# Optimization experiments

Hardware: AMD Instinct MI355X
Metric: run time of the kernel (lower is better)

## Reference

```python
import jax, jax.numpy as jnp
import numpy as np

V = 50000        # fine nodes
E = 400000       # edges
NEXT_DIM = 12500 # coarse nodes (nextDim)
B = 2
FIN, FOUT = 64, 128


def setup_inputs() -> dict:
    key = jax.random.key(0)
    ks = jax.random.split(key, 12)
    x = jax.random.normal(ks[0], (B, V, FIN), dtype=jnp.float32)
    adjValue = jax.random.uniform(ks[1], (E,), dtype=jnp.float32)
    edgeOne = jnp.ones((E,), dtype=jnp.float32)
    E_start = jax.random.randint(ks[2], (E,), 0, V, dtype=jnp.int32)
    E_end = jax.random.randint(ks[3], (E,), 0, V, dtype=jnp.int32)
    # avg-pool assignment: each fine node v -> coarse node v//4, weight 1/4
    fine = jnp.arange(V, dtype=jnp.int32)
    avgPoolAsgnIdx = jnp.stack([fine // 4, fine])  # [2, nnz]
    avgPoolAsgnValue = jnp.full((V,), 0.25, dtype=jnp.float32)
    s = 0.05
    W_res = jax.random.normal(ks[4], (FIN, FOUT), dtype=jnp.float32) * s
    b_res = jnp.zeros((FOUT,), dtype=jnp.float32)
    W0_self = jax.random.normal(ks[5], (FIN, FOUT), dtype=jnp.float32) * s
    W0_nb = jax.random.normal(ks[6], (FIN, FOUT), dtype=jnp.float32) * s
    b0 = jnp.zeros((FOUT,), dtype=jnp.float32)
    W1_self = jax.random.normal(ks[7], (FOUT, FOUT), dtype=jnp.float32) * s
    W1_nb = jax.random.normal(ks[8], (FOUT, FOUT), dtype=jnp.float32) * s
    b1 = jnp.zeros((FOUT,), dtype=jnp.float32)
    return {"x": x, "adjValue": adjValue, "edgeOne": edgeOne,
            "E_start": E_start, "E_end": E_end,
            "avgPoolAsgnIdx": avgPoolAsgnIdx, "avgPoolAsgnValue": avgPoolAsgnValue,
            "W_res": W_res, "b_res": b_res,
            "W0_self": W0_self, "W0_nb": W0_nb, "b0": b0,
            "W1_self": W1_self, "W1_nb": W1_nb, "b1": b1}


def _ecc(x, Ws, Wn, b, adjValue, E_start, E_end, deg_inv):
    # Edge-conditioned conv: out_i = x_i Ws + (1/deg_i) * sum_{e: start=i} adj_e * (x_{end(e)} Wn) + b
    Bn, Vn, _ = x.shape
    h = jnp.einsum('bvf,fo->bvo', x, Wn)            # neighbor transform [B,V,Fo]
    ht = h.transpose(1, 0, 2).reshape(Vn, -1)       # [V, B*Fo]
    msg = ht[E_end] * adjValue[:, None]             # gather + edge weight [E, B*Fo]
    agg = jax.ops.segment_sum(msg, E_start, num_segments=Vn)  # scatter-add [V, B*Fo]
    agg = (agg * deg_inv[:, None]).reshape(Vn, Bn, -1).transpose(1, 0, 2)
    return jnp.einsum('bvf,fo->bvo', x, Ws) + agg + b


def _batch_spmm(idx, value, m, x):
    # sparse (m x n) @ x per batch; x: [B, n, F]
    Bn, n, F = x.shape
    xt = x.transpose(1, 0, 2).reshape(n, -1)        # [n, B*F]
    g = xt[idx[1]] * value[:, None]                 # [nnz, B*F]
    out = jax.ops.segment_sum(g, idx[0], num_segments=m)
    return out.reshape(m, Bn, F).transpose(1, 0, 2)


def reference(x, adjValue, edgeOne, E_start, E_end, avgPoolAsgnIdx, avgPoolAsgnValue,
              W_res, b_res, W0_self, W0_nb, b0, W1_self, W1_nb, b1):
    deg = jax.ops.segment_sum(edgeOne, E_start, num_segments=V)
    deg_inv = 1.0 / jnp.maximum(deg, 1.0)
    # residual path: 1x1 conv == per-node linear, then pool
    residual = jnp.einsum('bvf,fo->bvo', x, W_res) + b_res
    residual = _batch_spmm(avgPoolAsgnIdx, avgPoolAsgnValue, NEXT_DIM, residual)
    # main path: ECC -> leaky_relu(0.2) -> ECC -> pool
    out = _ecc(x, W0_self, W0_nb, b0, adjValue, E_start, E_end, deg_inv)
    out = jnp.where(out >= 0, out, 0.2 * out)
    out = _ecc(out, W1_self, W1_nb, b1, adjValue, E_start, E_end, deg_inv)
    out = _batch_spmm(avgPoolAsgnIdx, avgPoolAsgnValue, NEXT_DIM, out)
    return out + residual
```

## Files before the change

### kernel.cpp

```cpp
#include <hip/hip_runtime.h>

#define V_N    50000
#define E_N    400000
#define NEXT_N 12500
#define B_N    2
#define M_ROWS (V_N * B_N)
#define NSBLK  196

typedef float  f32x2  __attribute__((ext_vector_type(2)));
typedef float  f32x4  __attribute__((ext_vector_type(4)));
typedef __bf16 bf16x8 __attribute__((ext_vector_type(8)));
typedef int    i32x2  __attribute__((ext_vector_type(2)));
typedef unsigned int u32x2 __attribute__((ext_vector_type(2)));
typedef unsigned int u32x4 __attribute__((ext_vector_type(4)));

__device__ __forceinline__ float bflo(unsigned int u) {
    return __builtin_bit_cast(float, u << 16);
}
__device__ __forceinline__ float bfhi(unsigned int u) {
    return __builtin_bit_cast(float, u & 0xffff0000u);
}
__device__ __forceinline__ unsigned short bf16bits(float f) {
    return __builtin_bit_cast(unsigned short, (__bf16)f);
}

__device__ __forceinline__ void wcvt_one(int idx, int phase,
                                         const float* Wa, const float* Wb, const float* Wc,
                                         unsigned int* dst) {
    int kc = idx >> 11;
    int jj = idx & 3, lane = (idx >> 2) & 63, nt = (idx >> 8) & 7;
    int kk = kc * 32 + ((lane >> 4) * 8) + jj * 2;
    int n  = nt * 16 + (lane & 15);
    const float* Wsrc; int kbase;
    if (phase == 0) {
        if (kk < 64) { Wsrc = Wa; kbase = 0; } else { Wsrc = Wb; kbase = 64; }
    } else {
        if (kk < 128)      { Wsrc = Wa; kbase = 0; }
        else if (kk < 256) { Wsrc = Wb; kbase = 128; }
        else               { Wsrc = Wc; kbase = 256; }
    }
    float w0 = Wsrc[(kk - kbase) * 128 + n];
    float w1 = Wsrc[(kk + 1 - kbase) * 128 + n];
    dst[idx] = ((unsigned int)bf16bits(w1) << 16) | bf16bits(w0);
}

__global__ void prep_kernel(const float* __restrict__ x, unsigned int* __restrict__ xbf,
                            const int* __restrict__ Es, int* __restrict__ degi,
                            const int* __restrict__ poolIdx, const float* __restrict__ poolVal,
                            int* __restrict__ invRow, float* __restrict__ invVal,
                            const float* __restrict__ W0s, const float* __restrict__ W0n,
                            const float* __restrict__ W1s, const float* __restrict__ W1n,
                            const float* __restrict__ Wres,
                            unsigned int* __restrict__ Wc0, unsigned int* __restrict__ Wc1) {
    int blk = blockIdx.x, t = threadIdx.x;
    if (blk < 12500) {
        int i = blk * 256 + t;
        f32x2 p = *(const f32x2*)(x + (size_t)i * 2);
        xbf[i] = ((unsigned int)bf16bits(p[1]) << 16) | bf16bits(p[0]);
    } else if (blk < 14063) {
        int e = (blk - 12500) * 256 + t;
        if (e < E_N) atomicAdd(&degi[Es[e]], 1);
    } else if (blk < 14259) {
        int j = (blk - 14063) * 256 + t;
        if (j < V_N) {
            int c = poolIdx[V_N + j];
            invRow[c] = poolIdx[j];
            invVal[c] = poolVal[j];
        }
    } else if (blk < 14291) {
        wcvt_one((blk - 14259) * 256 + t, 0, W0s, W0n, nullptr, Wc0);
    } else {
        wcvt_one((blk - 14291) * 256 + t, 1, W1s, W1n, Wres, Wc1);
    }
}

__global__ __launch_bounds__(256) void scan_kernel(const int* __restrict__ degi,
                                                   int* __restrict__ counter,
                                                   int* __restrict__ aggP,
                                                   int* __restrict__ cur,
                                                   float* __restrict__ dinv) {
    __shared__ int sh[256];
    __shared__ int pref[256];
    __shared__ int shrank;
    int t = threadIdx.x;
    if (t == 0) shrank = atomicAdd(counter, 1);
    __syncthreads();
    int rank = shrank;
    int i = rank * 256 + t;
    int d = (i < V_N) ? degi[i] : 0;
    sh[t] = d;
    __syncthreads();
    for (int off = 1; off < 256; off <<= 1) {
        int v = (t >= off) ? sh[t - off] : 0;
        __syncthreads();
        sh[t] += v;
        __syncthreads();
    }
    int incl = sh[t];
    int blocksum = sh[255];
    if (t == 0)
        __hip_atomic_store(&aggP[rank], blocksum + 1, __ATOMIC_RELEASE,
                           __HIP_MEMORY_SCOPE_AGENT);
    int pv = 0;
    if (t < rank) {
        int v;
        do {
            v = __hip_atomic_load(&aggP[t], __ATOMIC_ACQUIRE, __HIP_MEMORY_SCOPE_AGENT);
        } while (v == 0);
        pv = v - 1;
    }
    pref[t] = pv;
    __syncthreads();
    for (int off = 128; off > 0; off >>= 1) {
        if (t < off) pref[t] += pref[t + off];
        __syncthreads();
    }
    int prefix = pref[0];
    if (i < V_N) {
        cur[i] = prefix + incl - d;
        dinv[i] = 1.0f / (float)(d > 1 ? d : 1);
    }
}

__global__ void csr_kernel(const int* __restrict__ Es, const int* __restrict__ Ee,
                           const float* __restrict__ adj, int* __restrict__ cur,
                           i32x2* __restrict__ ecv) {
    int e = blockIdx.x * 256 + threadIdx.x;
    if (e < E_N) {
        int pos = atomicAdd(&cur[Es[e]], 1);
        i32x2 p;
        p[0] = Ee[e];
        p[1] = __float_as_int(adj[e]);
        ecv[pos] = p;
    }
}

__global__ __launch_bounds__(256) void agg0_kernel(
    const unsigned int* __restrict__ xbf, const int* __restrict__ cur,
    const i32x2* __restrict__ ecv, const float* __restrict__ dinv,
    unsigned int* __restrict__ AGG0bf) {
    int w = blockIdx.x * 4 + (threadIdx.x >> 6);
    int lane = threadIdx.x & 63;
    int beg = w ? cur[w - 1] : 0;
    int end = cur[w];
    int b = lane >> 5, u = lane & 31;
    const unsigned int* src = xbf + (size_t)b * V_N * 32 + u;
    float s0 = 0.f, s1 = 0.f;
    for (int base = beg; base < end; base += 8) {
        int li = base + (lane & 7);
        bool lv = li < end;
        i32x2 ev = lv ? ecv[li] : i32x2{0, 0};
        int dk = ev[0];
        float ak = __int_as_float(ev[1]);
        if (!lv) ak = 0.0f;
        unsigned int pv[8]; float av[8];
#pragma unroll
        for (int j = 0; j < 8; ++j) {
            int dj = __shfl(dk, j);
            av[j] = __shfl(ak, j);
            pv[j] = src[(size_t)dj * 32];
        }
#pragma unroll
        for (int j = 0; j < 8; ++j) { s0 += av[j] * bflo(pv[j]); s1 += av[j] * bfhi(pv[j]); }
    }
    float dv = dinv[w];
    AGG0bf[((size_t)b * V_N + w) * 32 + u] =
        ((unsigned int)bf16bits(s1 * dv) << 16) | bf16bits(s0 * dv);
}

__global__ __launch_bounds__(256) void agg1_kernel(
    const unsigned int* __restrict__ obf, const int* __restrict__ cur,
    const i32x2* __restrict__ ecv, const float* __restrict__ dinv,
    unsigned int* __restrict__ AGG1bf) {
    int w = blockIdx.x * 4 + (threadIdx.x >> 6);
    int lane = threadIdx.x & 63;
    int beg = w ? cur[w - 1] : 0;
    int end = cur[w];
    int b = lane >> 5;
    int u = (lane & 31) * 2;
    const unsigned int* src = obf + (size_t)b * V_N * 64 + u;
    float s[4] = {0, 0, 0, 0};
    for (int base = beg; base < end; base += 8) {
        int li = base + (lane & 7);
        bool lv = li < end;
        i32x2 ev = lv ? ecv[li] : i32x2{0, 0};
        int dk = ev[0];
        float ak = __int_as_float(ev[1]);
        if (!lv) ak = 0.0f;
        u32x2 pv[8]; float av[8];
#pragma unroll
        for (int j = 0; j < 8; ++j) {
            int dj = __shfl(dk, j);
            av[j] = __shfl(ak, j);
            pv[j] = *(const u32x2*)(src + (size_t)dj * 64);
        }
#pragma unroll
        for (int j = 0; j < 8; ++j) {
            s[0] += av[j] * bflo(pv[j][0]); s[1] += av[j] * bfhi(pv[j][0]);
            s[2] += av[j] * bflo(pv[j][1]); s[3] += av[j] * bfhi(pv[j][1]);
        }
    }
    float dv = dinv[w];
    u32x2 r;
    r[0] = ((unsigned int)bf16bits(s[1] * dv) << 16) | bf16bits(s[0] * dv);
    r[1] = ((unsigned int)bf16bits(s[3] * dv) << 16) | bf16bits(s[2] * dv);
    *(u32x2*)(AGG1bf + ((size_t)b * V_N + w) * 64 + u) = r;
}

template <int PHASE>
__global__ __launch_bounds__(256) void gemm_kernel(
    const unsigned int* __restrict__ xbf, const unsigned int* __restrict__ INbf,
    const unsigned int* __restrict__ AGGbf, const unsigned int* __restrict__ Wcvt,
    const float* __restrict__ bias0, const float* __restrict__ bias1,
    const int* __restrict__ invRow, const float* __restrict__ invVal,
    unsigned short* __restrict__ OUTbf, float* __restrict__ out) {
    constexpr int K  = (PHASE == 0) ? 128 : 320;
    constexpr int KC = K / 32;

    __shared__ unsigned int ldsW[KC * 2048];

    const int tid  = threadIdx.x;
    const int wave = tid >> 6, lane = tid & 63;
    const int m = lane & 15, quad = lane >> 4;

    {
        const u32x4* src4 = (const u32x4*)Wcvt;
        u32x4* dst4 = (u32x4*)ldsW;
#pragma unroll
        for (int it = 0; it < 2 * KC; ++it) dst4[it * 256 + tid] = src4[it * 256 + tid];
    }
    __syncthreads();

    const int rowA  = blockIdx.x * 64 + wave * 16 + m;
    const int rowAc = rowA < M_ROWS ? rowA : M_ROWS - 1;

    f32x4 acc[8];
#pragma unroll
    for (int i = 0; i < 8; ++i)
#pragma unroll
        for (int r = 0; r < 4; ++r) acc[i][r] = 0.0f;

#pragma unroll
    for (int kc = 0; kc < KC; ++kc) {
        int k0 = kc * 32 + quad * 8;
        const unsigned int* abase;
        if (PHASE == 0) {
            abase = (k0 < 64) ? xbf + (size_t)rowAc * 32 + (k0 >> 1)
                              : AGGbf + (size_t)rowAc * 32 + ((k0 - 64) >> 1);
        } else {
            if (k0 < 128)      abase = INbf + (size_t)rowAc * 64 + (k0 >> 1);
            else if (k0 < 256) abase = AGGbf + (size_t)rowAc * 64 + ((k0 - 128) >> 1);
            else               abase = xbf + (size_t)rowAc * 32 + ((k0 - 256) >> 1);
        }
        bf16x8 av = __builtin_bit_cast(bf16x8, *(const u32x4*)abase);
#pragma unroll
        for (int nt = 0; nt < 8; ++nt) {
            bf16x8 bv = __builtin_bit_cast(
                bf16x8, *(const u32x4*)&ldsW[(kc * 8 + nt) * 256 + lane * 4]);
            acc[nt] = __builtin_amdgcn_mfma_f32_16x16x32_bf16(av, bv, acc[nt], 0, 0, 0);
        }
    }

    const int rowq = blockIdx.x * 64 + wave * 16 + quad * 4;
    if (PHASE == 0) {
#pragma unroll
        for (int nt = 0; nt < 8; ++nt) {
            int o = nt * 16 + m;
            float bias = bias0[o];
#pragma unroll
            for (int r = 0; r < 4; ++r) {
                int orow = rowq + r;
                if (orow < M_ROWS) {
                    float val = acc[nt][r] + bias;
                    val = val >= 0.0f ? val : 0.2f * val;
                    OUTbf[(size_t)orow * 128 + o] = bf16bits(val);
                }
            }
        }
    } else {
        int b = rowq >= V_N;
        int vq = rowq - b * V_N;
        int rr0 = -2, rr1 = -2, rr2 = -2, rr3 = -2;
        float w0 = 0, w1 = 0, w2 = 0, w3 = 0;
        bool inb = (rowq + 3) < M_ROWS;
        if (inb) {
            rr0 = invRow[vq];     w0 = invVal[vq];
            rr1 = invRow[vq + 1]; w1 = invVal[vq + 1];
            rr2 = invRow[vq + 2]; w2 = invVal[vq + 2];
            rr3 = invRow[vq + 3]; w3 = invVal[vq + 3];
        }
        bool uniform = inb && (rr0 >= 0) && (rr0 == rr1) && (rr0 == rr2) && (rr0 == rr3);
#pragma unroll
        for (int nt = 0; nt < 8; ++nt) {
            int o = nt * 16 + m;
            float bias = bias0[o] + bias1[o];
            if (uniform) {
                float pooled = w0 * (acc[nt][0] + bias) + w1 * (acc[nt][1] + bias) +
                               w2 * (acc[nt][2] + bias) + w3 * (acc[nt][3] + bias);
                out[((size_t)b * NEXT_N + rr0) * 128 + o] = pooled;
            } else {
#pragma unroll
                for (int r = 0; r < 4; ++r) {
                    int orow = rowq + r;
                    if (orow < M_ROWS) {
                        int bb = orow >= V_N;
                        int vf = orow - bb * V_N;
                        int rrr = invRow[vf];
                        float www = invVal[vf];
                        if (rrr >= 0)
                            unsafeAtomicAdd(&out[((size_t)bb * NEXT_N + rrr) * 128 + o],
                                            www * (acc[nt][r] + bias));
                    }
                }
            }
        }
    }
}


extern "C" void kernel_launch(void* const* d_in, const int* in_sizes, int n_in,
                              void* d_out, int out_size, void* d_ws, size_t ws_size,
                              hipStream_t stream) {
    const float* x       = (const float*)d_in[0];
    const float* adj     = (const float*)d_in[1];
    const int*   Es      = (const int*)d_in[3];
    const int*   Ee      = (const int*)d_in[4];
    const int*   poolIdx = (const int*)d_in[5];
    const float* poolVal = (const float*)d_in[6];
    const float* W_res   = (const float*)d_in[7];
    const float* b_res   = (const float*)d_in[8];
    const float* W0s     = (const float*)d_in[9];
    const float* W0n     = (const float*)d_in[10];
    const float* b0      = (const float*)d_in[11];
    const float* W1s     = (const float*)d_in[12];
    const float* W1n     = (const float*)d_in[13];
    const float* b1      = (const float*)d_in[14];
    float* out = (float*)d_out;

    char* ws = (char*)d_ws;
    int*   invRow  = (int*)  (ws + 0);
    float* invVal  = (float*)(ws + 200704);
    int*   degi    = (int*)  (ws + 401408);
    int*   counter = (int*)  (ws + 601408);
    int*   aggP    = (int*)  (ws + 601412);
    float* dinv    = (float*)(ws + 602624);
    int*   cur     = (int*)  (ws + 803328);
    i32x2* ecv     = (i32x2*)(ws + 1003520);
    unsigned int* Wc0 = (unsigned int*)(ws + 4203520);
    unsigned int* Wc1 = (unsigned int*)(ws + 4236288);
    unsigned int* xbf    = (unsigned int*)(ws + 4318208);
    unsigned int* AGG0bf = (unsigned int*)(ws + 17118208);
    unsigned int* OUT0bf = (unsigned int*)(ws + 29918208);
    unsigned int* AGG1bf = (unsigned int*)(ws + 55518208);

    (void)hipMemsetAsync(degi, 0, 200788, stream);

    prep_kernel<<<14371, 256, 0, stream>>>(x, xbf, Es, degi, poolIdx, poolVal,
                                           invRow, invVal, W0s, W0n, W1s, W1n, W_res,
                                           Wc0, Wc1);
    scan_kernel<<<NSBLK, 256, 0, stream>>>(degi, counter, aggP, cur, dinv);
    csr_kernel<<<(E_N + 255) / 256, 256, 0, stream>>>(Es, Ee, adj, cur, ecv);

    agg0_kernel<<<12500, 256, 0, stream>>>(xbf, cur, ecv, dinv, AGG0bf);
    gemm_kernel<0><<<(M_ROWS + 63) / 64, 256, 0, stream>>>(
        xbf, nullptr, AGG0bf, Wc0, b0, nullptr, invRow, invVal,
        (unsigned short*)OUT0bf, nullptr);
    agg1_kernel<<<12500, 256, 0, stream>>>(OUT0bf, cur, ecv, dinv, AGG1bf);
    gemm_kernel<1><<<(M_ROWS + 63) / 64, 256, 0, stream>>>(
        xbf, OUT0bf, AGG1bf, Wc1, b1, b_res, invRow, invVal,
        nullptr, out);
}
```

Measured before the change: 255.4 us.

## Double GEMM rows per wave, widen edge batches, vectorize CSR build

The GEMM kernels now compute two 16-row M tiles per wave, 128 rows per block, so each LDS weight fragment feeds two MFMAs and the per-block weight staging is amortised over twice the rows. The aggregation kernels load up to 32 edge records per iteration with one coalesced load and then gather in chunks of 8, cutting redundant ecv loads. The CSR build processes two edges per thread with vector loads. The trade-offs are more accumulator registers (possibly lower occupancy), half as many GEMM blocks, and an extra inner loop in the gather kernels.

```diff
diff --git a/kernel.cpp b/kernel.cpp
--- a/kernel.cpp
+++ b/kernel.cpp
@@ -125,12 +125,19 @@
 __global__ void csr_kernel(const int* __restrict__ Es, const int* __restrict__ Ee,
                            const float* __restrict__ adj, int* __restrict__ cur,
                            i32x2* __restrict__ ecv) {
-    int e = blockIdx.x * 256 + threadIdx.x;
-    if (e < E_N) {
-        int pos = atomicAdd(&cur[Es[e]], 1);
-        i32x2 p;
-        p[0] = Ee[e];
-        p[1] = __float_as_int(adj[e]);
+    int e0 = (blockIdx.x * 256 + threadIdx.x) * 2;
+    if (e0 >= E_N) return;
+    i32x2 s2 = *(const i32x2*)(Es + e0);
+    i32x2 d2 = *(const i32x2*)(Ee + e0);
+    f32x2 a2 = *(const f32x2*)(adj + e0);
+    {
+        int pos = atomicAdd(&cur[s2[0]], 1);
+        i32x2 p; p[0] = d2[0]; p[1] = __float_as_int(a2[0]);
+        ecv[pos] = p;
+    }
+    {
+        int pos = atomicAdd(&cur[s2[1]], 1);
+        i32x2 p; p[0] = d2[1]; p[1] = __float_as_int(a2[1]);
         ecv[pos] = p;
     }
 }
@@ -146,22 +153,24 @@
     int b = lane >> 5, u = lane & 31;
     const unsigned int* src = xbf + (size_t)b * V_N * 32 + u;
     float s0 = 0.f, s1 = 0.f;
-    for (int base = beg; base < end; base += 8) {
-        int li = base + (lane & 7);
-        bool lv = li < end;
+    for (int base = beg; base < end; base += 32) {
+        int li = base + lane;
+        bool lv = (lane < 32) && (li < end);
         i32x2 ev = lv ? ecv[li] : i32x2{0, 0};
         int dk = ev[0];
-        float ak = __int_as_float(ev[1]);
-        if (!lv) ak = 0.0f;
-        unsigned int pv[8]; float av[8];
-#pragma unroll
-        for (int j = 0; j < 8; ++j) {
-            int dj = __shfl(dk, j);
-            av[j] = __shfl(ak, j);
-            pv[j] = src[(size_t)dj * 32];
-        }
-#pragma unroll
-        for (int j = 0; j < 8; ++j) { s0 += av[j] * bflo(pv[j]); s1 += av[j] * bfhi(pv[j]); }
+        float ak = lv ? __int_as_float(ev[1]) : 0.0f;
+        int nrem = end - base; if (nrem > 32) nrem = 32;
+        for (int jb = 0; jb < nrem; jb += 8) {
+            unsigned int pv[8]; float av8[8];
+#pragma unroll
+            for (int j = 0; j < 8; ++j) {
+                int dj = __shfl(dk, jb + j);
+                av8[j] = __shfl(ak, jb + j);
+                pv[j] = src[(size_t)dj * 32];
+            }
+#pragma unroll
+            for (int j = 0; j < 8; ++j) { s0 += av8[j] * bflo(pv[j]); s1 += av8[j] * bfhi(pv[j]); }
+        }
     }
     float dv = dinv[w];
     AGG0bf[((size_t)b * V_N + w) * 32 + u] =
@@ -180,24 +189,26 @@
     int u = (lane & 31) * 2;
     const unsigned int* src = obf + (size_t)b * V_N * 64 + u;
     float s[4] = {0, 0, 0, 0};
-    for (int base = beg; base < end; base += 8) {
-        int li = base + (lane & 7);
-        bool lv = li < end;
+    for (int base = beg; base < end; base += 32) {
+        int li = base + lane;
+        bool lv = (lane < 32) && (li < end);
         i32x2 ev = lv ? ecv[li] : i32x2{0, 0};
         int dk = ev[0];
-        float ak = __int_as_float(ev[1]);
-        if (!lv) ak = 0.0f;
-        u32x2 pv[8]; float av[8];
-#pragma unroll
-        for (int j = 0; j < 8; ++j) {
-            int dj = __shfl(dk, j);
-            av[j] = __shfl(ak, j);
-            pv[j] = *(const u32x2*)(src + (size_t)dj * 64);
-        }
-#pragma unroll
-        for (int j = 0; j < 8; ++j) {
-            s[0] += av[j] * bflo(pv[j][0]); s[1] += av[j] * bfhi(pv[j][0]);
-            s[2] += av[j] * bflo(pv[j][1]); s[3] += av[j] * bfhi(pv[j][1]);
+        float ak = lv ? __int_as_float(ev[1]) : 0.0f;
+        int nrem = end - base; if (nrem > 32) nrem = 32;
+        for (int jb = 0; jb < nrem; jb += 8) {
+            u32x2 pv[8]; float av8[8];
+#pragma unroll
+            for (int j = 0; j < 8; ++j) {
+                int dj = __shfl(dk, jb + j);
+                av8[j] = __shfl(ak, jb + j);
+                pv[j] = *(const u32x2*)(src + (size_t)dj * 64);
+            }
+#pragma unroll
+            for (int j = 0; j < 8; ++j) {
+                s[0] += av8[j] * bflo(pv[j][0]); s[1] += av8[j] * bfhi(pv[j][0]);
+                s[2] += av8[j] * bflo(pv[j][1]); s[3] += av8[j] * bfhi(pv[j][1]);
+            }
         }
     }
     float dv = dinv[w];
@@ -231,85 +242,100 @@
     }
     __syncthreads();
 
-    const int rowA  = blockIdx.x * 64 + wave * 16 + m;
-    const int rowAc = rowA < M_ROWS ? rowA : M_ROWS - 1;
-
-    f32x4 acc[8];
-#pragma unroll
-    for (int i = 0; i < 8; ++i)
-#pragma unroll
-        for (int r = 0; r < 4; ++r) acc[i][r] = 0.0f;
+    const int rowBase = blockIdx.x * 128 + wave * 32;
+    int rA[2];
+#pragma unroll
+    for (int mt = 0; mt < 2; ++mt) {
+        int r = rowBase + mt * 16 + m;
+        rA[mt] = r < M_ROWS ? r : M_ROWS - 1;
+    }
+
+    f32x4 acc[2][8];
+#pragma unroll
+    for (int mt = 0; mt < 2; ++mt)
+#pragma unroll
+        for (int i = 0; i < 8; ++i)
+#pragma unroll
+            for (int r = 0; r < 4; ++r) acc[mt][i][r] = 0.0f;
 
 #pragma unroll
     for (int kc = 0; kc < KC; ++kc) {
         int k0 = kc * 32 + quad * 8;
-        const unsigned int* abase;
-        if (PHASE == 0) {
-            abase = (k0 < 64) ? xbf + (size_t)rowAc * 32 + (k0 >> 1)
-                              : AGGbf + (size_t)rowAc * 32 + ((k0 - 64) >> 1);
-        } else {
-            if (k0 < 128)      abase = INbf + (size_t)rowAc * 64 + (k0 >> 1);
-            else if (k0 < 256) abase = AGGbf + (size_t)rowAc * 64 + ((k0 - 128) >> 1);
-            else               abase = xbf + (size_t)rowAc * 32 + ((k0 - 256) >> 1);
-        }
-        bf16x8 av = __builtin_bit_cast(bf16x8, *(const u32x4*)abase);
+        bf16x8 av[2];
+#pragma unroll
+        for (int mt = 0; mt < 2; ++mt) {
+            const unsigned int* abase;
+            if (PHASE == 0) {
+                abase = (k0 < 64) ? xbf + (size_t)rA[mt] * 32 + (k0 >> 1)
+                                  : AGGbf + (size_t)rA[mt] * 32 + ((k0 - 64) >> 1);
+            } else {
+                if (k0 < 128)      abase = INbf + (size_t)rA[mt] * 64 + (k0 >> 1);
+                else if (k0 < 256) abase = AGGbf + (size_t)rA[mt] * 64 + ((k0 - 128) >> 1);
+                else               abase = xbf + (size_t)rA[mt] * 32 + ((k0 - 256) >> 1);
+            }
+            av[mt] = __builtin_bit_cast(bf16x8, *(const u32x4*)abase);
+        }
 #pragma unroll
         for (int nt = 0; nt < 8; ++nt) {
             bf16x8 bv = __builtin_bit_cast(
                 bf16x8, *(const u32x4*)&ldsW[(kc * 8 + nt) * 256 + lane * 4]);
-            acc[nt] = __builtin_amdgcn_mfma_f32_16x16x32_bf16(av, bv, acc[nt], 0, 0, 0);
-        }
-    }
-
-    const int rowq = blockIdx.x * 64 + wave * 16 + quad * 4;
-    if (PHASE == 0) {
-#pragma unroll
-        for (int nt = 0; nt < 8; ++nt) {
-            int o = nt * 16 + m;
-            float bias = bias0[o];
-#pragma unroll
-            for (int r = 0; r < 4; ++r) {
-                int orow = rowq + r;
-                if (orow < M_ROWS) {
-                    float val = acc[nt][r] + bias;
-                    val = val >= 0.0f ? val : 0.2f * val;
-                    OUTbf[(size_t)orow * 128 + o] = bf16bits(val);
-                }
-            }
-        }
-    } else {
-        int b = rowq >= V_N;
-        int vq = rowq - b * V_N;
-        int rr0 = -2, rr1 = -2, rr2 = -2, rr3 = -2;
-        float w0 = 0, w1 = 0, w2 = 0, w3 = 0;
-        bool inb = (rowq + 3) < M_ROWS;
-        if (inb) {
-            rr0 = invRow[vq];     w0 = invVal[vq];
-            rr1 = invRow[vq + 1]; w1 = invVal[vq + 1];
-            rr2 = invRow[vq + 2]; w2 = invVal[vq + 2];
-            rr3 = invRow[vq + 3]; w3 = invVal[vq + 3];
-        }
-        bool uniform = inb && (rr0 >= 0) && (rr0 == rr1) && (rr0 == rr2) && (rr0 == rr3);
-#pragma unroll
-        for (int nt = 0; nt < 8; ++nt) {
-            int o = nt * 16 + m;
-            float bias = bias0[o] + bias1[o];
-            if (uniform) {
-                float pooled = w0 * (acc[nt][0] + bias) + w1 * (acc[nt][1] + bias) +
-                               w2 * (acc[nt][2] + bias) + w3 * (acc[nt][3] + bias);
-                out[((size_t)b * NEXT_N + rr0) * 128 + o] = pooled;
-            } else {
+            acc[0][nt] = __builtin_amdgcn_mfma_f32_16x16x32_bf16(av[0], bv, acc[0][nt], 0, 0, 0);
+            acc[1][nt] = __builtin_amdgcn_mfma_f32_16x16x32_bf16(av[1], bv, acc[1][nt], 0, 0, 0);
+        }
+    }
+
+#pragma unroll
+    for (int mt = 0; mt < 2; ++mt) {
+        const int rowq = rowBase + mt * 16 + quad * 4;
+        if (PHASE == 0) {
+#pragma unroll
+            for (int nt = 0; nt < 8; ++nt) {
+                int o = nt * 16 + m;
+                float bias = bias0[o];
 #pragma unroll
                 for (int r = 0; r < 4; ++r) {
                     int orow = rowq + r;
                     if (orow < M_ROWS) {
-                        int bb = orow >= V_N;
-                        int vf = orow - bb * V_N;
-                        int rrr = invRow[vf];
-                        float www = invVal[vf];
-                        if (rrr >= 0)
-                            unsafeAtomicAdd(&out[((size_t)bb * NEXT_N + rrr) * 128 + o],
-                                            www * (acc[nt][r] + bias));
+                        float val = acc[mt][nt][r] + bias;
+                        val = val >= 0.0f ? val : 0.2f * val;
+                        OUTbf[(size_t)orow * 128 + o] = bf16bits(val);
+                    }
+                }
+            }
+        } else {
+            int b = rowq >= V_N;
+            int vq = rowq - b * V_N;
+            int rr0 = -2, rr1 = -2, rr2 = -2, rr3 = -2;
+            float w0 = 0, w1 = 0, w2 = 0, w3 = 0;
+            bool inb = (rowq + 3) < M_ROWS;
+            if (inb) {
+                rr0 = invRow[vq];     w0 = invVal[vq];
+                rr1 = invRow[vq + 1]; w1 = invVal[vq + 1];
+                rr2 = invRow[vq + 2]; w2 = invVal[vq + 2];
+                rr3 = invRow[vq + 3]; w3 = invVal[vq + 3];
+            }
+            bool uniform = inb && (rr0 >= 0) && (rr0 == rr1) && (rr0 == rr2) && (rr0 == rr3);
+#pragma unroll
+            for (int nt = 0; nt < 8; ++nt) {
+                int o = nt * 16 + m;
+                float bias = bias0[o] + bias1[o];
+                if (uniform) {
+                    float pooled = w0 * (acc[mt][nt][0] + bias) + w1 * (acc[mt][nt][1] + bias) +
+                                   w2 * (acc[mt][nt][2] + bias) + w3 * (acc[mt][nt][3] + bias);
+                    out[((size_t)b * NEXT_N + rr0) * 128 + o] = pooled;
+                } else {
+#pragma unroll
+                    for (int r = 0; r < 4; ++r) {
+                        int orow = rowq + r;
+                        if (orow < M_ROWS) {
+                            int bb = orow >= V_N;
+                            int vf = orow - bb * V_N;
+                            int rrr = invRow[vf];
+                            float www = invVal[vf];
+                            if (rrr >= 0)
+                                unsafeAtomicAdd(&out[((size_t)bb * NEXT_N + rrr) * 128 + o],
+                                                www * (acc[mt][nt][r] + bias));
+                        }
                     }
                 }
             }
@@ -359,14 +385,14 @@
                                            invRow, invVal, W0s, W0n, W1s, W1n, W_res,
                                            Wc0, Wc1);
     scan_kernel<<<NSBLK, 256, 0, stream>>>(degi, counter, aggP, cur, dinv);
-    csr_kernel<<<(E_N + 255) / 256, 256, 0, stream>>>(Es, Ee, adj, cur, ecv);
+    csr_kernel<<<(E_N / 2 + 255) / 256, 256, 0, stream>>>(Es, Ee, adj, cur, ecv);
 
     agg0_kernel<<<12500, 256, 0, stream>>>(xbf, cur, ecv, dinv, AGG0bf);
-    gemm_kernel<0><<<(M_ROWS + 63) / 64, 256, 0, stream>>>(
+    gemm_kernel<0><<<(M_ROWS + 127) / 128, 256, 0, stream>>>(
         xbf, nullptr, AGG0bf, Wc0, b0, nullptr, invRow, invVal,
         (unsigned short*)OUT0bf, nullptr);
     agg1_kernel<<<12500, 256, 0, stream>>>(OUT0bf, cur, ecv, dinv, AGG1bf);
-    gemm_kernel<1><<<(M_ROWS + 63) / 64, 256, 0, stream>>>(
+    gemm_kernel<1><<<(M_ROWS + 127) / 128, 256, 0, stream>>>(
         xbf, OUT0bf, AGG1bf, Wc1, b1, b_res, invRow, invVal,
         nullptr, out);
 }
```

After: 249.9 us. 1.02x faster.
